# Kernel tuning notes

Hardware: AMD Instinct MI355X
Metric: run time of the kernel (lower is better)

## Reference

```python
import jax, jax.numpy as jnp
import numpy as np

ALPHA = 1.0

def setup_inputs() -> dict:
    key = jax.random.key(0)
    kx, kd = jax.random.split(key)
    B, L, D = 64, 256, 512
    x = jax.random.normal(kx, (B, L, D), dtype=jnp.float32)
    duration = jax.random.randint(kd, (B, L), 0, 8, dtype=jnp.int32)
    max_length = 1792  # L * max_duration
    return {"x": x, "duration": duration, "max_length": max_length}

def reference(x, duration, max_length):
    B, L, D = x.shape
    # round(duration * alpha) -> integer durations
    d = jnp.round(duration.astype(jnp.float32) * ALPHA).astype(jnp.int32)
    # rows with all-zero durations get one frame (original picks a random
    # position; we deterministically use position 0)
    row_sum = d.sum(axis=1)  # [B]
    d = jnp.where((row_sum == 0)[:, None] & (jnp.arange(L) == 0)[None, :], 1, d)
    # cumulative end offsets per phoneme: cum[b, j] = sum_{k<=j} d[b, k]
    cum = jnp.cumsum(d, axis=1)  # [B, L]
    t = jnp.arange(max_length)   # [T]
    # output frame t belongs to phoneme j where cum[j-1] <= t < cum[j]
    idx = jax.vmap(lambda c: jnp.searchsorted(c, t, side='right'))(cum)  # [B, T]
    idx = jnp.clip(idx, 0, L - 1)
    out = jnp.take_along_axis(x, idx[:, :, None], axis=1)  # [B, T, D]
    # zero-pad beyond each sequence's total length
    mask = (t[None, :] < cum[:, -1:]).astype(x.dtype)  # [B, T]
    out = out * mask[:, :, None]
    return out, max_length
```

## Files before the change

### kernel.cpp

```cpp
#include <hip/hip_runtime.h>


#define BB 64
#define LL 256
#define DD 512
#define TT 1792
#define D4 (DD / 4)
#define TILE 64
#define NBT (TT / TILE)
#define NBLK (BB * NBT)

typedef float f32x4 __attribute__((ext_vector_type(4)));

__global__ __launch_bounds__(256) void length_regulator_kernel(
    const f32x4* __restrict__ x4,
    const int*   __restrict__ dur,
    const int*   __restrict__ maxlen,
    float*       __restrict__ out)
{
    __shared__ int cum[LL];
    __shared__ int idx_s[TILE];
    const int tid = threadIdx.x;

    const int bid  = blockIdx.x;
    const int virt = (bid & 7) * (NBLK / 8) + (bid >> 3);
    const int b    = virt / NBT;
    const int t0   = (virt % NBT) * TILE;

    cum[tid] = dur[b * LL + tid];
    if (tid < TILE) idx_s[tid] = -1;
    __syncthreads();
    #pragma unroll
    for (int off = 1; off < LL; off <<= 1) {
        int v = (tid >= off) ? cum[tid - off] : 0;
        __syncthreads();
        cum[tid] += v;
        __syncthreads();
    }
    if (cum[LL - 1] == 0) cum[tid] = 1;
    __syncthreads();

    {
        const int end   = cum[tid];
        const int start = (tid > 0) ? cum[tid - 1] : 0;
        const int lo = max(start, t0);
        const int hi = min(end, t0 + TILE);
        for (int t = lo; t < hi; ++t) idx_s[t - t0] = tid;
    }
    __syncthreads();

    const int group = tid >> 7;
    const int lane  = tid & 127;
    const f32x4 z   = (f32x4)(0.f);
    const f32x4* __restrict__ xrow = x4 + (size_t)b * LL * D4;
    f32x4* __restrict__ outb = (f32x4*)out + ((size_t)b * TT + t0) * D4;

    #pragma unroll
    for (int itb = 0; itb < TILE / 2; itb += 4) {
        const int ta = (itb + 0) * 2 + group;
        const int tb = (itb + 1) * 2 + group;
        const int tc = (itb + 2) * 2 + group;
        const int td = (itb + 3) * 2 + group;
        const int ia = idx_s[ta];
        const int ib = idx_s[tb];
        const int ic = idx_s[tc];
        const int ie = idx_s[td];
        f32x4 va = xrow[max(ia, 0) * D4 + lane];
        f32x4 vb = xrow[max(ib, 0) * D4 + lane];
        f32x4 vc = xrow[max(ic, 0) * D4 + lane];
        f32x4 ve = xrow[max(ie, 0) * D4 + lane];
        va = (ia >= 0) ? va : z;
        vb = (ib >= 0) ? vb : z;
        vc = (ic >= 0) ? vc : z;
        ve = (ie >= 0) ? ve : z;
        outb[ta * D4 + lane] = va;
        outb[tb * D4 + lane] = vb;
        outb[tc * D4 + lane] = vc;
        outb[td * D4 + lane] = ve;
    }

    if (virt == 0 && tid == 0) {
        out[(size_t)BB * TT * DD] = (float)maxlen[0];
    }
}

extern "C" void kernel_launch(void* const* d_in, const int* in_sizes, int n_in,
                              void* d_out, int out_size, void* d_ws, size_t ws_size,
                              hipStream_t stream) {
    const f32x4* x4  = (const f32x4*)d_in[0];
    const int*   dur = (const int*)d_in[1];
    const int*   ml  = (const int*)d_in[2];
    float*       out = (float*)d_out;

    length_regulator_kernel<<<dim3(NBLK), dim3(256), 0, stream>>>(x4, dur, ml, out);
}
```

Before: 264.3 us.

## Split scan into separate kernel writing frame indices to workspace

Adds a per-batch scan/scatter kernel that computes the frame-to-phoneme index map once and writes it to workspace, followed by a copy kernel that reads those indices instead of redoing the 256-element prefix scan in every tile block. This removes the redundant scan (28 times per batch) and its barriers from the bandwidth-bound copy. In exchange it adds a second launch, a small global index array round-trip, and a serial dependency between kernels. The fused kernel is kept as a fallback when no workspace is available.

Result: no change. 267.5 us (+1.2%).

```diff
diff --git a/kernel.cpp b/kernel.cpp
--- a/kernel.cpp
+++ b/kernel.cpp
@@ -12,16 +12,91 @@
 
 typedef float f32x4 __attribute__((ext_vector_type(4)));
 
-__global__ __launch_bounds__(256) void length_regulator_kernel(
+__global__ __launch_bounds__(256) void scan_scatter_kernel(
+    const int* __restrict__ dur,
+    const int* __restrict__ maxlen,
+    int*       __restrict__ idx_g,
+    float*     __restrict__ out)
+{
+    __shared__ int cum[LL];
+    const int tid = threadIdx.x;
+    const int b   = blockIdx.x;
+
+    cum[tid] = dur[b * LL + tid];
+    __syncthreads();
+    #pragma unroll
+    for (int off = 1; off < LL; off <<= 1) {
+        int v = (tid >= off) ? cum[tid - off] : 0;
+        __syncthreads();
+        cum[tid] += v;
+        __syncthreads();
+    }
+    if (cum[LL - 1] == 0) cum[tid] = 1;
+    __syncthreads();
+
+    int* idxb = idx_g + b * TT;
+    #pragma unroll
+    for (int t = tid; t < TT; t += 256) idxb[t] = -1;
+    __syncthreads();
+    {
+        const int end   = cum[tid];
+        const int start = (tid > 0) ? cum[tid - 1] : 0;
+        for (int t = start; t < end; ++t) idxb[t] = tid;
+    }
+
+    if (b == 0 && tid == 0) out[(size_t)BB * TT * DD] = (float)maxlen[0];
+}
+
+__global__ __launch_bounds__(256) void copy_kernel(
     const f32x4* __restrict__ x4,
-    const int*   __restrict__ dur,
-    const int*   __restrict__ maxlen,
+    const int*   __restrict__ idx_g,
     float*       __restrict__ out)
+{
+    const int bid  = blockIdx.x;
+    const int virt = (bid & 7) * (NBLK / 8) + (bid >> 3);
+    const int b    = virt / NBT;
+    const int t0   = (virt % NBT) * TILE;
+
+    const int tid   = threadIdx.x;
+    const int group = tid >> 7;
+    const int lane  = tid & 127;
+    const f32x4 z   = (f32x4)(0.f);
+    const f32x4* __restrict__ xrow = x4 + (size_t)b * LL * D4;
+    const int*   __restrict__ idxb = idx_g + b * TT + t0;
+    f32x4* __restrict__ outb = (f32x4*)out + ((size_t)b * TT + t0) * D4;
+
+    #pragma unroll
+    for (int itb = 0; itb < TILE / 2; itb += 4) {
+        const int ta = (itb + 0) * 2 + group;
+        const int tb = (itb + 1) * 2 + group;
+        const int tc = (itb + 2) * 2 + group;
+        const int td = (itb + 3) * 2 + group;
+        const int ia = idxb[ta];
+        const int ib = idxb[tb];
+        const int ic = idxb[tc];
+        const int ie = idxb[td];
+        f32x4 va = xrow[max(ia, 0) * D4 + lane];
+        f32x4 vb = xrow[max(ib, 0) * D4 + lane];
+        f32x4 vc = xrow[max(ic, 0) * D4 + lane];
+        f32x4 ve = xrow[max(ie, 0) * D4 + lane];
+        va = (ia >= 0) ? va : z;
+        vb = (ib >= 0) ? vb : z;
+        vc = (ic >= 0) ? vc : z;
+        ve = (ie >= 0) ? ve : z;
+        outb[ta * D4 + lane] = va;
+        outb[tb * D4 + lane] = vb;
+        outb[tc * D4 + lane] = vc;
+        outb[td * D4 + lane] = ve;
+    }
+}
+
+__global__ __launch_bounds__(256) void length_regulator_fused(
+    const f32x4* __restrict__ x4, const int* __restrict__ dur,
+    const int* __restrict__ maxlen, float* __restrict__ out)
 {
     __shared__ int cum[LL];
     __shared__ int idx_s[TILE];
     const int tid = threadIdx.x;
-
     const int bid  = blockIdx.x;
     const int virt = (bid & 7) * (NBLK / 8) + (bid >> 3);
     const int b    = virt / NBT;
@@ -39,7 +114,6 @@
     }
     if (cum[LL - 1] == 0) cum[tid] = 1;
     __syncthreads();
-
     {
         const int end   = cum[tid];
         const int start = (tid > 0) ? cum[tid - 1] : 0;
@@ -78,10 +152,7 @@
         outb[tc * D4 + lane] = vc;
         outb[td * D4 + lane] = ve;
     }
-
-    if (virt == 0 && tid == 0) {
-        out[(size_t)BB * TT * DD] = (float)maxlen[0];
-    }
+    if (virt == 0 && tid == 0) out[(size_t)BB * TT * DD] = (float)maxlen[0];
 }
 
 extern "C" void kernel_launch(void* const* d_in, const int* in_sizes, int n_in,
@@ -92,5 +163,12 @@
     const int*   ml  = (const int*)d_in[2];
     float*       out = (float*)d_out;
 
-    length_regulator_kernel<<<dim3(NBLK), dim3(256), 0, stream>>>(x4, dur, ml, out);
+    const size_t idx_bytes = (size_t)BB * TT * sizeof(int);
+    if (d_ws != nullptr && ws_size >= idx_bytes) {
+        int* idx_g = (int*)d_ws;
+        scan_scatter_kernel<<<dim3(BB), dim3(256), 0, stream>>>(dur, ml, idx_g, out);
+        copy_kernel<<<dim3(NBLK), dim3(256), 0, stream>>>(x4, idx_g, out);
+    } else {
+        length_regulator_fused<<<dim3(NBLK), dim3(256), 0, stream>>>(x4, dur, ml, out);
+    }
 }
```
